# Kernel tuning notes

Measured on AMD Instinct MI355X. Metric: run time of the kernel, lower is better.

Reference implementation:

```python
import jax, jax.numpy as jnp
import numpy as np

R = 2.0            # distance exponent
Q = 1.0            # activation exponent
SPECIFICITY = 1.0  # c in exp(-c * dist)
BETA = 3.0         # lateral competition exponent
TEMP_COMP = 1.0    # ClusterCompetition temperature
TEMP_WTA = 0.1     # SoftWTA temperature
PHI = 1.5          # association scaling
NEG_INF = -1e30

B, C, D = 1024, 512, 256


def setup_inputs() -> dict:
    key = jax.random.key(0)
    k1, k2, k3, k4, k5 = jax.random.split(key, 5)
    inp = jax.random.normal(k1, (B, D), dtype=jnp.float32)
    w_dist = jax.random.normal(k2, (C, D), dtype=jnp.float32)      # cluster centers
    attn = jax.random.uniform(k3, (D,), dtype=jnp.float32)         # dim-wise attention (>=0)
    w_assoc = jax.random.normal(k4, (C, 2), dtype=jnp.float32)     # association weights
    mask = jax.random.randint(k5, (C,), 0, 2, dtype=jnp.int32)     # recruited-cluster mask
    return {"inp": inp, "w_dist": w_dist, "attn": attn, "w_assoc": w_assoc, "mask": mask}


def reference(inp, w_dist, attn, w_assoc, mask):
    m = mask.astype(inp.dtype)                       # [C] 0/1 recruited gate
    # Distance: per-dim |x - w|^r for every (item, cluster) pair -> [B, C, D]
    dim_dist = jnp.abs(inp[:, None, :] - w_dist[None, :, :]) ** R
    # DimWiseAttention: sum-to-one constrained attention over dims
    a = attn / jnp.sum(attn)
    # ClusterActivation: H_j = exp(-c * (sum_d a_d * dist_d)^(q/r)) -> [B, C]
    wdist = jnp.einsum('bcd,d->bc', dim_dist, a)
    H = jnp.exp(-SPECIFICITY * wdist ** (Q / R))
    clusters_actv = H * m                            # MaskNonRecruit
    nonzero = m > 0
    # ClusterCompetition: softmax over recruited clusters of actv^beta (temp-scaled),
    # re-weighting each cluster's own activation.
    comp_logits = jnp.where(nonzero, BETA * jnp.log(H) / TEMP_COMP, NEG_INF)
    p_comp = jax.nn.softmax(comp_logits, axis=-1)
    competed = p_comp * clusters_actv                # [B, C]
    # SoftWTA: plain temperature softmax over recruited clusters, same re-weighting.
    wta_logits = jnp.where(nonzero, competed / TEMP_WTA, NEG_INF)
    p_wta = jax.nn.softmax(wta_logits, axis=-1)
    softwta = p_wta * competed                       # [B, C]
    # Classification: Phi-scaled linear readout to 2 classes.
    y_pred = PHI * (softwta @ w_assoc)               # [B, 2]
    return y_pred
```

## Files before the change

### kernel.cpp

```cpp
#include <hip/hip_runtime.h>
#include <math.h>

#define BN 1024
#define CN 512
#define DN 256
#define ROWS 4
#define WAVES 8
#define KC (DN / WAVES)

#define XS_OFF 0
#define R_OFF  (BN * DN)
#define Q_OFF  (R_OFF + BN)

__launch_bounds__(256, 4)
__global__ void prep_kernel(const float* __restrict__ inp, const float* __restrict__ wd,
                            const float* __restrict__ attn, float* __restrict__ ws) {
    __shared__ float red[4];
    float* xs = ws + XS_OFF;
    float* r  = ws + R_OFF;
    float* q  = ws + Q_OFF;

    const int tid  = threadIdx.x;
    const int lane = tid & 63;
    const int blk  = blockIdx.x;

    float av = attn[tid];
    float s = av;
    #pragma unroll
    for (int off = 32; off > 0; off >>= 1) s += __shfl_xor(s, off);
    if (lane == 0) red[tid >> 6] = s;
    __syncthreads();
    const float a = av / (red[0] + red[1] + red[2] + red[3]);

    float c;
    if (blk < BN) {
        const float x = inp[blk * DN + tid];
        xs[blk * DN + tid] = a * x;
        c = a * x * x;
    } else {
        const float w = wd[(blk - BN) * DN + tid];
        c = a * w * w;
    }
    #pragma unroll
    for (int off = 32; off > 0; off >>= 1) c += __shfl_xor(c, off);
    __syncthreads();
    if (lane == 0) red[tid >> 6] = c;
    __syncthreads();
    if (tid == 0) {
        const float tot = red[0] + red[1] + red[2] + red[3];
        if (blk < BN) r[blk] = tot; else q[blk - BN] = tot;
    }
}

#define NEG_INF_F (-1e30f)

__device__ __forceinline__ float waveMax(float v) {
    #pragma unroll
    for (int off = 32; off > 0; off >>= 1) v = fmaxf(v, __shfl_xor(v, off));
    return v;
}
__device__ __forceinline__ float waveSum(float v) {
    #pragma unroll
    for (int off = 32; off > 0; off >>= 1) v += __shfl_xor(v, off);
    return v;
}

__launch_bounds__(512, 1)
__global__ void fused_kernel(const float* __restrict__ ws, const float* __restrict__ wd,
                             const int* __restrict__ mask, const float* __restrict__ w_assoc,
                             float* __restrict__ y) {
    __shared__ float red[WAVES * 32 * 64];

    const int tid  = threadIdx.x;
    const int lane = tid & 63;
    const int wz   = __builtin_amdgcn_readfirstlane(tid >> 6);
    const int b0   = blockIdx.x * ROWS;
    const int kbase = wz * KC;

    const float* xs = ws + XS_OFF;

    const float* wp[8];
    #pragma unroll
    for (int j = 0; j < 8; ++j)
        wp[j] = wd + (size_t)(lane + 64 * j) * DN + kbase;

    float acc[ROWS][8] = {};

    #pragma unroll
    for (int k4 = 0; k4 < KC / 4; ++k4) {
        float4 xv[ROWS];
        #pragma unroll
        for (int rr = 0; rr < ROWS; ++rr) {
            const int idx = __builtin_amdgcn_readfirstlane((b0 + rr) * DN + kbase + 4 * k4);
            xv[rr] = *(const float4*)&xs[idx];
        }
        #pragma unroll
        for (int j = 0; j < 8; ++j) {
            const float4 w4 = *(const float4*)(wp[j] + 4 * k4);
            #pragma unroll
            for (int rr = 0; rr < ROWS; ++rr) {
                float t = fmaf(xv[rr].x, w4.x, acc[rr][j]);
                t = fmaf(xv[rr].y, w4.y, t);
                t = fmaf(xv[rr].z, w4.z, t);
                acc[rr][j] = fmaf(xv[rr].w, w4.w, t);
            }
        }
    }

    #pragma unroll
    for (int rr = 0; rr < ROWS; ++rr)
        #pragma unroll
        for (int j = 0; j < 8; ++j)
            red[(wz * 32 + rr * 8 + j) * 64 + lane] = acc[rr][j];
    __syncthreads();

    if (wz < ROWS) {
        const int rr = wz;

        float dot[8] = {};
        #pragma unroll
        for (int z = 0; z < WAVES; ++z)
            #pragma unroll
            for (int j = 0; j < 8; ++j)
                dot[j] += red[(z * 32 + rr * 8 + j) * 64 + lane];

        const float rb = ws[R_OFF + b0 + rr];

        float t[8]; bool rec[8];
        #pragma unroll
        for (int j = 0; j < 8; ++j) {
            const int c = lane + 64 * j;
            const float wdist = fmaxf(rb + ws[Q_OFF + c] - 2.0f * dot[j], 0.0f);
            t[j] = sqrtf(wdist);
            rec[j] = mask[c] > 0;
        }

        float l1[8], lmax = NEG_INF_F;
        #pragma unroll
        for (int j = 0; j < 8; ++j) { l1[j] = rec[j] ? (-3.0f * t[j]) : NEG_INF_F; lmax = fmaxf(lmax, l1[j]); }
        const float mx1 = waveMax(lmax);
        float e1[8], lsum = 0.f;
        #pragma unroll
        for (int j = 0; j < 8; ++j) { e1[j] = rec[j] ? expf(l1[j] - mx1) : 0.f; lsum += e1[j]; }
        const float inv_s1 = 1.0f / waveSum(lsum);

        float competed[8];
        #pragma unroll
        for (int j = 0; j < 8; ++j) competed[j] = e1[j] * inv_s1 * expf(-t[j]);

        float l2[8]; lmax = NEG_INF_F;
        #pragma unroll
        for (int j = 0; j < 8; ++j) { l2[j] = rec[j] ? (competed[j] * 10.0f) : NEG_INF_F; lmax = fmaxf(lmax, l2[j]); }
        const float mx2 = waveMax(lmax);
        float e2[8]; lsum = 0.f;
        #pragma unroll
        for (int j = 0; j < 8; ++j) { e2[j] = rec[j] ? expf(l2[j] - mx2) : 0.f; lsum += e2[j]; }
        const float inv_s2 = 1.0f / waveSum(lsum);

        float y0 = 0.f, y1 = 0.f;
        #pragma unroll
        for (int j = 0; j < 8; ++j) {
            const int c = lane + 64 * j;
            const float sw = e2[j] * inv_s2 * competed[j];
            const float2 wa = *(const float2*)&w_assoc[2 * c];
            y0 = fmaf(sw, wa.x, y0);
            y1 = fmaf(sw, wa.y, y1);
        }
        y0 = waveSum(y0);
        y1 = waveSum(y1);
        if (lane == 0) {
            float2 o = {1.5f * y0, 1.5f * y1};
            *(float2*)&y[(b0 + rr) * 2] = o;
        }
    }
}

extern "C" void kernel_launch(void* const* d_in, const int* in_sizes, int n_in,
                              void* d_out, int out_size, void* d_ws, size_t ws_size,
                              hipStream_t stream) {
    const float* inp     = (const float*)d_in[0];
    const float* w_dist  = (const float*)d_in[1];
    const float* attn    = (const float*)d_in[2];
    const float* w_assoc = (const float*)d_in[3];
    const int*   mask    = (const int*)d_in[4];
    float* out = (float*)d_out;
    float* ws  = (float*)d_ws;

    prep_kernel<<<BN + CN, 256, 0, stream>>>(inp, w_dist, attn, ws);
    fused_kernel<<<BN / ROWS, 512, 0, stream>>>(ws, w_dist, mask, w_assoc, out);
}
```

Baseline: 87.83 us.

## Fuse prep into single kernel computing direct squared differences with LDS double-buffering

```diff
diff --git a/kernel.cpp b/kernel.cpp
--- a/kernel.cpp
+++ b/kernel.cpp
@@ -4,53 +4,10 @@
 #define BN 1024
 #define CN 512
 #define DN 256
-#define ROWS 4
-#define WAVES 8
-#define KC (DN / WAVES)
-
-#define XS_OFF 0
-#define R_OFF  (BN * DN)
-#define Q_OFF  (R_OFF + BN)
-
-__launch_bounds__(256, 4)
-__global__ void prep_kernel(const float* __restrict__ inp, const float* __restrict__ wd,
-                            const float* __restrict__ attn, float* __restrict__ ws) {
-    __shared__ float red[4];
-    float* xs = ws + XS_OFF;
-    float* r  = ws + R_OFF;
-    float* q  = ws + Q_OFF;
-
-    const int tid  = threadIdx.x;
-    const int lane = tid & 63;
-    const int blk  = blockIdx.x;
-
-    float av = attn[tid];
-    float s = av;
-    #pragma unroll
-    for (int off = 32; off > 0; off >>= 1) s += __shfl_xor(s, off);
-    if (lane == 0) red[tid >> 6] = s;
-    __syncthreads();
-    const float a = av / (red[0] + red[1] + red[2] + red[3]);
-
-    float c;
-    if (blk < BN) {
-        const float x = inp[blk * DN + tid];
-        xs[blk * DN + tid] = a * x;
-        c = a * x * x;
-    } else {
-        const float w = wd[(blk - BN) * DN + tid];
-        c = a * w * w;
-    }
-    #pragma unroll
-    for (int off = 32; off > 0; off >>= 1) c += __shfl_xor(c, off);
-    __syncthreads();
-    if (lane == 0) red[tid >> 6] = c;
-    __syncthreads();
-    if (tid == 0) {
-        const float tot = red[0] + red[1] + red[2] + red[3];
-        if (blk < BN) r[blk] = tot; else q[blk - BN] = tot;
-    }
-}
+#define RB 4
+#define KCH 16
+#define NCH (DN / KCH)
+#define WSTR 17
 
 #define NEG_INF_F (-1e30f)
 
@@ -65,113 +22,144 @@
     return v;
 }
 
-__launch_bounds__(512, 1)
-__global__ void fused_kernel(const float* __restrict__ ws, const float* __restrict__ wd,
-                             const int* __restrict__ mask, const float* __restrict__ w_assoc,
-                             float* __restrict__ y) {
-    __shared__ float red[WAVES * 32 * 64];
+__launch_bounds__(256, 1)
+__global__ void clus_kernel(const float* __restrict__ inp, const float* __restrict__ wd,
+                            const float* __restrict__ attn, const float* __restrict__ w_assoc,
+                            const int* __restrict__ mask, float* __restrict__ y) {
+    __shared__ __align__(16) float wbuf[2][CN * WSTR];
+    __shared__ __align__(16) float xs[RB][DN];
+    __shared__ __align__(16) float sarr[DN];
+    __shared__ float red4[4];
 
     const int tid  = threadIdx.x;
     const int lane = tid & 63;
     const int wz   = __builtin_amdgcn_readfirstlane(tid >> 6);
-    const int b0   = blockIdx.x * ROWS;
-    const int kbase = wz * KC;
+    const int b0   = blockIdx.x * RB;
 
-    const float* xs = ws + XS_OFF;
-
-    const float* wp[8];
+    const float av = attn[tid];
+    float ssum = av;
     #pragma unroll
-    for (int j = 0; j < 8; ++j)
-        wp[j] = wd + (size_t)(lane + 64 * j) * DN + kbase;
-
-    float acc[ROWS][8] = {};
+    for (int off = 32; off > 0; off >>= 1) ssum += __shfl_xor(ssum, off);
+    if (lane == 0) red4[wz] = ssum;
+    __syncthreads();
+    const float total = red4[0] + red4[1] + red4[2] + red4[3];
+    sarr[tid] = sqrtf(av / total);
+    __syncthreads();
 
     #pragma unroll
-    for (int k4 = 0; k4 < KC / 4; ++k4) {
-        float4 xv[ROWS];
+    for (int i = 0; i < RB; ++i)
+        xs[i][tid] = inp[(b0 + i) * DN + tid] * sarr[tid];
+
+    const int col4  = (tid & 3) * 4;
+    const int rbase = tid >> 2;
+
+    {
+        const float4 sv = *(const float4*)&sarr[col4];
         #pragma unroll
-        for (int rr = 0; rr < ROWS; ++rr) {
-            const int idx = __builtin_amdgcn_readfirstlane((b0 + rr) * DN + kbase + 4 * k4);
-            xv[rr] = *(const float4*)&xs[idx];
+        for (int p = 0; p < 8; ++p) {
+            const int row = rbase + 64 * p;
+            float4 w4 = *(const float4*)&wd[row * DN + col4];
+            w4.x *= sv.x; w4.y *= sv.y; w4.z *= sv.z; w4.w *= sv.w;
+            *(float4*)&wbuf[0][row * WSTR + col4] = w4;
         }
-        #pragma unroll
-        for (int j = 0; j < 8; ++j) {
-            const float4 w4 = *(const float4*)(wp[j] + 4 * k4);
+    }
+    __syncthreads();
+
+    float acc[RB][8] = {};
+    const int kk = wz << 2;
+
+    for (int z = 0; z < NCH; ++z) {
+        if (z + 1 < NCH) {
+            const int k0 = (z + 1) * KCH;
+            const float4 sv = *(const float4*)&sarr[k0 + col4];
+            float* dst = &wbuf[(z + 1) & 1][0];
             #pragma unroll
-            for (int rr = 0; rr < ROWS; ++rr) {
-                float t = fmaf(xv[rr].x, w4.x, acc[rr][j]);
-                t = fmaf(xv[rr].y, w4.y, t);
-                t = fmaf(xv[rr].z, w4.z, t);
-                acc[rr][j] = fmaf(xv[rr].w, w4.w, t);
+            for (int p = 0; p < 8; ++p) {
+                const int row = rbase + 64 * p;
+                float4 w4 = *(const float4*)&wd[row * DN + k0 + col4];
+                w4.x *= sv.x; w4.y *= sv.y; w4.z *= sv.z; w4.w *= sv.w;
+                *(float4*)&dst[row * WSTR + col4] = w4;
             }
         }
+        {
+            const float* wsrc = &wbuf[z & 1][0];
+            float4 xv[RB];
+            #pragma unroll
+            for (int rr = 0; rr < RB; ++rr)
+                xv[rr] = *(const float4*)&xs[rr][z * KCH + kk];
+            #pragma unroll
+            for (int j = 0; j < 8; ++j) {
+                const float4 w4 = *(const float4*)&wsrc[(lane + 64 * j) * WSTR + kk];
+                #pragma unroll
+                for (int rr = 0; rr < RB; ++rr) {
+                    float d0 = xv[rr].x - w4.x; acc[rr][j] = fmaf(d0, d0, acc[rr][j]);
+                    float d1 = xv[rr].y - w4.y; acc[rr][j] = fmaf(d1, d1, acc[rr][j]);
+                    float d2 = xv[rr].z - w4.z; acc[rr][j] = fmaf(d2, d2, acc[rr][j]);
+                    float d3 = xv[rr].w - w4.w; acc[rr][j] = fmaf(d3, d3, acc[rr][j]);
+                }
+            }
+        }
+        __syncthreads();
     }
 
+    float* comb = &wbuf[0][0];
     #pragma unroll
-    for (int rr = 0; rr < ROWS; ++rr)
+    for (int rr = 0; rr < RB; ++rr)
         #pragma unroll
         for (int j = 0; j < 8; ++j)
-            red[(wz * 32 + rr * 8 + j) * 64 + lane] = acc[rr][j];
+            comb[(wz * 32 + rr * 8 + j) * 64 + lane] = acc[rr][j];
     __syncthreads();
 
-    if (wz < ROWS) {
-        const int rr = wz;
+    const int rr = wz;
+    float dist[8] = {};
+    #pragma unroll
+    for (int zz = 0; zz < 4; ++zz)
+        #pragma unroll
+        for (int j = 0; j < 8; ++j)
+            dist[j] += comb[(zz * 32 + rr * 8 + j) * 64 + lane];
 
-        float dot[8] = {};
-        #pragma unroll
-        for (int z = 0; z < WAVES; ++z)
-            #pragma unroll
-            for (int j = 0; j < 8; ++j)
-                dot[j] += red[(z * 32 + rr * 8 + j) * 64 + lane];
+    float t[8]; bool rec[8];
+    #pragma unroll
+    for (int j = 0; j < 8; ++j) {
+        t[j] = sqrtf(dist[j]);
+        rec[j] = mask[lane + 64 * j] > 0;
+    }
 
-        const float rb = ws[R_OFF + b0 + rr];
+    float l1[8], lmax = NEG_INF_F;
+    #pragma unroll
+    for (int j = 0; j < 8; ++j) { l1[j] = rec[j] ? (-3.0f * t[j]) : NEG_INF_F; lmax = fmaxf(lmax, l1[j]); }
+    const float mx1 = waveMax(lmax);
+    float e1[8], lsum = 0.f;
+    #pragma unroll
+    for (int j = 0; j < 8; ++j) { e1[j] = rec[j] ? expf(l1[j] - mx1) : 0.f; lsum += e1[j]; }
+    const float inv_s1 = 1.0f / waveSum(lsum);
 
-        float t[8]; bool rec[8];
-        #pragma unroll
-        for (int j = 0; j < 8; ++j) {
-            const int c = lane + 64 * j;
-            const float wdist = fmaxf(rb + ws[Q_OFF + c] - 2.0f * dot[j], 0.0f);
-            t[j] = sqrtf(wdist);
-            rec[j] = mask[c] > 0;
-        }
+    float competed[8];
+    #pragma unroll
+    for (int j = 0; j < 8; ++j) competed[j] = e1[j] * inv_s1 * expf(-t[j]);
 
-        float l1[8], lmax = NEG_INF_F;
-        #pragma unroll
-        for (int j = 0; j < 8; ++j) { l1[j] = rec[j] ? (-3.0f * t[j]) : NEG_INF_F; lmax = fmaxf(lmax, l1[j]); }
-        const float mx1 = waveMax(lmax);
-        float e1[8], lsum = 0.f;
-        #pragma unroll
-        for (int j = 0; j < 8; ++j) { e1[j] = rec[j] ? expf(l1[j] - mx1) : 0.f; lsum += e1[j]; }
-        const float inv_s1 = 1.0f / waveSum(lsum);
+    float l2[8]; lmax = NEG_INF_F;
+    #pragma unroll
+    for (int j = 0; j < 8; ++j) { l2[j] = rec[j] ? (competed[j] * 10.0f) : NEG_INF_F; lmax = fmaxf(lmax, l2[j]); }
+    const float mx2 = waveMax(lmax);
+    float e2[8]; lsum = 0.f;
+    #pragma unroll
+    for (int j = 0; j < 8; ++j) { e2[j] = rec[j] ? expf(l2[j] - mx2) : 0.f; lsum += e2[j]; }
+    const float inv_s2 = 1.0f / waveSum(lsum);
 
-        float competed[8];
-        #pragma unroll
-        for (int j = 0; j < 8; ++j) competed[j] = e1[j] * inv_s1 * expf(-t[j]);
-
-        float l2[8]; lmax = NEG_INF_F;
-        #pragma unroll
-        for (int j = 0; j < 8; ++j) { l2[j] = rec[j] ? (competed[j] * 10.0f) : NEG_INF_F; lmax = fmaxf(lmax, l2[j]); }
-        const float mx2 = waveMax(lmax);
-        float e2[8]; lsum = 0.f;
-        #pragma unroll
-        for (int j = 0; j < 8; ++j) { e2[j] = rec[j] ? expf(l2[j] - mx2) : 0.f; lsum += e2[j]; }
-        const float inv_s2 = 1.0f / waveSum(lsum);
-
-        float y0 = 0.f, y1 = 0.f;
-        #pragma unroll
-        for (int j = 0; j < 8; ++j) {
-            const int c = lane + 64 * j;
-            const float sw = e2[j] * inv_s2 * competed[j];
-            const float2 wa = *(const float2*)&w_assoc[2 * c];
-            y0 = fmaf(sw, wa.x, y0);
-            y1 = fmaf(sw, wa.y, y1);
-        }
-        y0 = waveSum(y0);
-        y1 = waveSum(y1);
-        if (lane == 0) {
-            float2 o = {1.5f * y0, 1.5f * y1};
-            *(float2*)&y[(b0 + rr) * 2] = o;
-        }
+    float y0 = 0.f, y1 = 0.f;
+    #pragma unroll
+    for (int j = 0; j < 8; ++j) {
+        const float sw = e2[j] * inv_s2 * competed[j];
+        const float2 wa = *(const float2*)&w_assoc[2 * (lane + 64 * j)];
+        y0 = fmaf(sw, wa.x, y0);
+        y1 = fmaf(sw, wa.y, y1);
+    }
+    y0 = waveSum(y0);
+    y1 = waveSum(y1);
+    if (lane == 0) {
+        float2 o = {1.5f * y0, 1.5f * y1};
+        *(float2*)&y[(b0 + rr) * 2] = o;
     }
 }
 
@@ -184,8 +172,6 @@
     const float* w_assoc = (const float*)d_in[3];
     const int*   mask    = (const int*)d_in[4];
     float* out = (float*)d_out;
-    float* ws  = (float*)d_ws;
 
-    prep_kernel<<<BN + CN, 256, 0, stream>>>(inp, w_dist, attn, ws);
-    fused_kernel<<<BN / ROWS, 512, 0, stream>>>(ws, w_dist, mask, w_assoc, out);
+    clus_kernel<<<BN / RB, 256, 0, stream>>>(inp, w_dist, attn, w_assoc, mask, out);
 }
```

Result: slower. 101.1 us (+15.1%).
